# Kernel tuning notes

Hardware: AMD Instinct MI355X
Metric: run time of the kernel (lower is better)

Reference implementation:

```python
import jax, jax.numpy as jnp
import numpy as np

N, B = 1024, 32
PEP_PAD, L, M, E, VOCAB = 3, 27, 34, 16, 26
CN, KS, OFFS = (128, 256, 256), (3, 5, 7), (2, 1, 0)
LIN = (512, 256)
BN_EPS = 1e-5


def _pe(length, d):
    pos = np.arange(length, dtype=np.float32)[:, None]
    div = np.exp(np.arange(0, d, 2, dtype=np.float32) * (-np.log(10000.0) / d))
    pe = np.zeros((length, d), np.float32)
    pe[:, 0::2] = np.sin(pos * div)
    pe[:, 1::2] = np.cos(pos * div)
    return jnp.asarray(pe)

PE_MHC = _pe(M, E)
PE_PEP = _pe(100, E)[: L - 2 * PEP_PAD]


def _bn(x, g, b):
    # inference-mode BatchNorm2d (running_mean=0, running_var=1)
    s = g / jnp.sqrt(1.0 + BN_EPS)
    return x * s[None, :, None, None] + b[None, :, None, None]


def _iconv(pep, mhc, W, b):
    # interaction conv: pep (N, Lin, E, S), mhc (N, M, E), W (C, K, M)
    # out[n,c,i,s] = sum_{k,m,e} W[c,k,m] * mhc[n,m,e] * pep[n,i+k,e,s] + b[c]
    K = W.shape[1]
    Kb = jnp.einsum('ckm,nme->ncke', W, mhc)  # per-sample kernel (N,C,K,E)
    Lout = pep.shape[1] - K + 1
    out = sum(jnp.einsum('nce,nies->ncis', Kb[:, :, k], pep[:, k:k + Lout]) for k in range(K))
    return out + b[None, :, None, None]


def _fwd(params, peptide_x, mhc_x, bags_size, inverse):
    (emb_pep, emb_mhc, convs_f, convs_r, lins_f, lins_r,
     w_att1, b_att1, w_att2, b_att2, w_out, b_out) = params
    masks = peptide_x[:, PEP_PAD:L - PEP_PAD] != 0              # (N, 21)
    mhc_e = emb_mhc[mhc_x] + PE_MHC                             # (N, 34, E)
    pep_e = emb_pep[peptide_x]
    pep_e = jnp.concatenate([pep_e[:, :PEP_PAD],
                             pep_e[:, PEP_PAD:L - PEP_PAD] + PE_PEP,
                             pep_e[:, L - PEP_PAD:]], axis=1)    # (N, 27, E)
    pep_c = pep_e[..., None]                                     # (N,27,E,1)
    pep_i = jnp.stack([pep_e[:, ::-1], pep_e], axis=-1)          # (N,27,E,2)

    def branch(pep, convs, inversion):
        outs = []
        for (W, bb, g, be), off in zip(convs, OFFS):
            Wk = W[:, ::-1] if inversion else W
            x = _iconv(pep[:, off:L - off], mhc_e, Wk, bb)
            outs.append(jax.nn.relu(_bn(x, g, be)))
        return jnp.concatenate(outs, axis=1)

    conv_out = branch(pep_c, convs_f, False)                     # (N, 640, 21, 1)
    conv_r = branch(pep_i, convs_r, True)                        # (N, 640, 21, 2)
    conv_r = jnp.concatenate([conv_r[..., 0:1][:, :, ::-1], conv_r[..., 1:2]], axis=-1)

    def mlp(x, lins):
        for Wl, bl, gl, bel in lins:
            x = jax.nn.relu(_bn(jnp.einsum('oc,nciw->noiw', Wl, x) + bl[None, :, None, None], gl, bel))
        return x

    conv_out = mlp(conv_out, lins_f)                             # (N, 256, 21, 1)
    conv_r = mlp(conv_r, lins_r)                                 # (N, 256, 21, 2)
    x = jnp.concatenate([conv_out, conv_r], axis=-1)             # (N, 256, 21, 3)
    m = masks[:, None, -x.shape[2]:, None]
    pool = jnp.max(jnp.where(m, x, -jnp.inf), axis=2, keepdims=True)  # (N,256,1,3)

    # attention MIL over variable-size bags (segment softmax)
    feat = pool.mean(axis=(2, 3))                                # (N, 256)
    a = (jnp.tanh(feat @ w_att1.T + b_att1) @ w_att2.T + b_att2)[:, 0]
    nb = bags_size.shape[0]
    seg = jnp.repeat(jnp.arange(nb), bags_size, total_repeat_length=feat.shape[0])
    amax = jax.lax.stop_gradient(jax.ops.segment_max(a, seg, num_segments=nb))
    ex = jnp.exp(a - amax[seg])
    att = ex / jax.ops.segment_sum(ex, seg, num_segments=nb)[seg]

    score = jax.nn.sigmoid(jnp.einsum('oc,nciw->noiw', w_out, pool) + b_out[None, :, None, None])  # (N,2,1,3)
    half = score[..., :2].sum(-1) * 0.5
    if inverse:
        s = jnp.stack([half, score[..., -1]], axis=-1)           # (N,2,1,2)
    else:
        s = jnp.stack([half, half], axis=-1)
    s = s.max(axis=-1)                                           # (N, 2, 1)
    if inverse:
        s = jax.ops.segment_sum(att[:, None, None] * s, seg, num_segments=nb)  # (B,2,1)
    else:
        s = s.sum(axis=-1) * 0.5
    s = jnp.clip(s, 0.0, 1.0)
    return s.reshape(s.shape[0], -1)                             # (B, 2)


def setup_inputs() -> dict:
    key = jax.random.key(0)
    ks = iter(jax.random.split(key, 64))
    nrm = lambda shape, std=0.02: jax.random.normal(next(ks), shape, jnp.float32) * std
    d = {}
    d['peptide_x'] = jax.random.randint(next(ks), (N, L), 1, VOCAB)
    d['mhc_x'] = jax.random.randint(next(ks), (N, M), 1, VOCAB)
    d['context_x'] = jax.random.randint(next(ks), (N, 12), 1, VOCAB)
    d['peptide_esm_x'] = jnp.zeros((N, 2, 10, 3), jnp.float32)
    d['bags_size'] = jnp.full((B,), N // B, jnp.int32)
    d['inverse'] = 1
    d['emb_pep'] = jax.random.uniform(next(ks), (VOCAB, E), jnp.float32, -0.1, 0.1)
    d['emb_mhc'] = jax.random.uniform(next(ks), (VOCAB, E), jnp.float32, -0.1, 0.1)
    for tag in ('cf', 'cr'):
        for j, (c, k) in enumerate(zip(CN, KS)):
            d[f'w_{tag}{j}'] = nrm((c, k, M), 0.05)
            d[f'b_{tag}{j}'] = jnp.zeros((c,), jnp.float32)
            d[f'g_{tag}{j}'] = 1.0 + nrm((c,), 0.002)
            d[f'be_{tag}{j}'] = jnp.zeros((c,), jnp.float32)
    dims = [sum(CN)] + list(LIN)
    for tag in ('lf', 'lr'):
        for j, (i_s, o_s) in enumerate(zip(dims[:-1], dims[1:])):
            d[f'w_{tag}{j}'] = nrm((o_s, i_s), 0.02)
            d[f'b_{tag}{j}'] = jnp.zeros((o_s,), jnp.float32)
            d[f'g_{tag}{j}'] = 1.0 + nrm((o_s,), 0.002)
            d[f'be_{tag}{j}'] = jnp.zeros((o_s,), jnp.float32)
    H = LIN[-1]
    d['w_att1'] = nrm((H, H)); d['b_att1'] = jnp.zeros((H,), jnp.float32)
    d['w_att2'] = nrm((1, H)); d['b_att2'] = jnp.zeros((1,), jnp.float32)
    d['w_out'] = nrm((2, H), 0.1); d['b_out'] = jnp.zeros((2,), jnp.float32)
    return d


def reference(peptide_x, mhc_x, context_x, peptide_esm_x, bags_size, inverse,
              emb_pep, emb_mhc,
              w_cf0, b_cf0, g_cf0, be_cf0, w_cf1, b_cf1, g_cf1, be_cf1, w_cf2, b_cf2, g_cf2, be_cf2,
              w_cr0, b_cr0, g_cr0, be_cr0, w_cr1, b_cr1, g_cr1, be_cr1, w_cr2, b_cr2, g_cr2, be_cr2,
              w_lf0, b_lf0, g_lf0, be_lf0, w_lf1, b_lf1, g_lf1, be_lf1,
              w_lr0, b_lr0, g_lr0, be_lr0, w_lr1, b_lr1, g_lr1, be_lr1,
              w_att1, b_att1, w_att2, b_att2, w_out, b_out):
    convs_f = [(w_cf0, b_cf0, g_cf0, be_cf0), (w_cf1, b_cf1, g_cf1, be_cf1), (w_cf2, b_cf2, g_cf2, be_cf2)]
    convs_r = [(w_cr0, b_cr0, g_cr0, be_cr0), (w_cr1, b_cr1, g_cr1, be_cr1), (w_cr2, b_cr2, g_cr2, be_cr2)]
    lins_f = [(w_lf0, b_lf0, g_lf0, be_lf0), (w_lf1, b_lf1, g_lf1, be_lf1)]
    lins_r = [(w_lr0, b_lr0, g_lr0, be_lr0), (w_lr1, b_lr1, g_lr1, be_lr1)]
    params = (emb_pep, emb_mhc, convs_f, convs_r, lins_f, lins_r,
              w_att1, b_att1, w_att2, b_att2, w_out, b_out)
    return _fwd(params, peptide_x, mhc_x, bags_size, int(inverse))
```

## Files before the change

kernel.cpp:

```cpp
#include <hip/hip_runtime.h>
#include <hip/hip_bf16.h>
#include <math.h>

#define NS   1024
#define LP   27
#define MMH  34
#define EE   16
#define LO   21
#define CT   640
#define H1   512
#define H2   256
#define LPAD 40
#define GROW (LP*LPAD)
#define SLOTROWS (NS*LO)
#define ALLROWS  (3*SLOTROWS)

typedef __attribute__((ext_vector_type(8))) short  s8v;
typedef __attribute__((ext_vector_type(4))) float  f4v;

#define PK2_SLOT 147456
#define PK2_J0   0
#define PK2_J1   16384
#define PK2_J2   73728
#define WMLP_FAM 458752
#define WMLP_B   327680
#define BMLP_FAM 768
#define BMLP_B   512

__device__ __forceinline__ ushort f2b(float v) {
    __hip_bfloat16 hb = __float2bfloat16(v);
    return *reinterpret_cast<ushort*>(&hb);
}

__device__ __forceinline__ float pe_val(int pos, int e) {
    int j = e >> 1;
    float div = expf(-1.1512925464970229f * (float)j);
    float ang = (float)pos * div;
    return (e & 1) ? cosf(ang) : sinf(ang);
}

__device__ __forceinline__ int xcd_swz() {
    int fid = blockIdx.y * gridDim.x + blockIdx.x;
    int nwg = gridDim.x * gridDim.y;
    int cpx = nwg >> 3;
    return (fid & 7) * cpx + (fid >> 3);
}

struct PrepArgs {
    const int* pep_x; const int* mhc_x;
    const float* emb_pep; const float* emb_mhc;
    const float* cw[2][3]; const float* cb[2][3]; const float* cg[2][3]; const float* cbe[2][3];
    const float* mw[4]; const float* mb[4]; const float* mg[4]; const float* mbe[4];
    ushort* Gb; ushort* Wpack; float* bpack; ushort* Wmlp; float* bmlp; int* poolI;
};

__global__ __launch_bounds__(256) void k_prep(PrepArgs A) {
    int b = blockIdx.x, t = threadIdx.x;
    float rs = rsqrtf(1.0f + 1e-5f);
    if (b < NS) {
        __shared__ float ps[LP * 17];
        __shared__ float ms[MMH * 17];
        int n = b;
        for (int idx = t; idx < LP * EE; idx += 256) {
            int l = idx >> 4, e = idx & 15;
            float v = A.emb_pep[A.pep_x[n * LP + l] * EE + e];
            if (l >= 3 && l < 24) v += pe_val(l - 3, e);
            ps[l * 17 + e] = v;
        }
        for (int idx = t; idx < MMH * EE; idx += 256) {
            int m = idx >> 4, e = idx & 15;
            ms[m * 17 + e] = A.emb_mhc[A.mhc_x[n * MMH + m] * EE + e] + pe_val(m, e);
        }
        __syncthreads();
        for (int idx = t; idx < GROW; idx += 256) {
            int l = idx / LPAD, m = idx - l * LPAD;
            float s = 0.f;
            if (m < MMH) {
                #pragma unroll
                for (int e = 0; e < EE; ++e) s = fmaf(ps[l * 17 + e], ms[m * 17 + e], s);
            }
            A.Gb[(size_t)n * GROW + idx] = f2b(s);
        }
        if (n == 0 && t < 64) A.Gb[(size_t)NS * GROW + t] = 0;
    } else if (b < NS + 144) {
        const int KS_[3]  = {3, 5, 7};
        const int KCP_[3] = {128, 224, 288};
        const int NC_[3]  = {128, 256, 256};
        const int pkoff[3] = {PK2_J0, PK2_J1, PK2_J2};
        const int bpoff[3] = {0, 128, 384};
        int lin = b - NS;
        int s = lin / 48, rem = lin - s * 48, j = rem >> 4, z = rem & 15;
        int K = KS_[j], Kcp = KCP_[j], nc = NC_[j];
        int fam = (s == 0) ? 0 : 1;
        const float* w  = A.cw[fam][j];
        const float* g  = A.cg[fam][j];
        ushort* Wp = A.Wpack + s * PK2_SLOT + pkoff[j];
        int tot = nc * Kcp;
        for (int idx = z * 256 + t; idx < tot; idx += 16 * 256) {
            int c = idx / Kcp, col = idx - c * Kcp;
            int k = col / LPAD, m = col - k * LPAD;
            float v = 0.f;
            if (k < K && m < MMH) {
                int kk = (s == 2) ? (K - 1 - k) : k;
                v = w[((size_t)c * K + kk) * MMH + m] * (g[c] * rs);
            }
            Wp[idx] = f2b(v);
        }
        if (z == 0) {
            const float* bb = A.cb[fam][j];
            const float* be = A.cbe[fam][j];
            float* bp = A.bpack + s * CT + bpoff[j];
            for (int c = t; c < nc; c += 256)
                bp[c] = bb[c] * (g[c] * rs) + be[c];
        }
    } else if (b < NS + 144 + 112) {
        int lin = b - NS - 144;
        int task, rel, nb;
        if (lin < 40)      { task = 0; rel = lin;      nb = 40; }
        else if (lin < 56) { task = 1; rel = lin - 40; nb = 16; }
        else if (lin < 96) { task = 2; rel = lin - 56; nb = 40; }
        else               { task = 3; rel = lin - 96; nb = 16; }
        int fam = task >> 1, stage = task & 1;
        int Co = stage ? H2 : H1;
        int Ci = stage ? H1 : CT;
        const float* w  = A.mw[task];
        const float* g  = A.mg[task];
        ushort* Wb = A.Wmlp + fam * WMLP_FAM + stage * WMLP_B;
        int tot = Co * Ci;
        for (int idx = rel * 256 + t; idx < tot; idx += nb * 256) {
            int o = idx / Ci;
            Wb[idx] = f2b(w[idx] * (g[o] * rs));
        }
        if (rel == 0) {
            const float* bb = A.mb[task];
            const float* be = A.mbe[task];
            float* bp = A.bmlp + fam * BMLP_FAM + stage * BMLP_B;
            for (int o = t; o < Co; o += 256)
                bp[o] = bb[o] * (g[o] * rs) + be[o];
        }
    } else {
        int base = (b - NS - 144 - 112) * 8192;
        #pragma unroll
        for (int q = 0; q < 32; ++q)
            A.poolI[base + q * 256 + t] = 0;
    }
}

__global__ __launch_bounds__(512) void k_cmfma(
    const ushort* __restrict__ Gb, const ushort* __restrict__ Wpack,
    const float* __restrict__ bpack, ushort* __restrict__ Xb, int rowBase)
{
    const int kcpm[5] = {128, 224, 224, 288, 288};
    const int offm[5] = {2, 1, 1, 0, 0};
    const int o0m[5]  = {0, 0, 128, 0, 128};
    const int c0m[5]  = {0, 128, 128, 384, 384};
    const int wofm[5] = {PK2_J0, PK2_J1, PK2_J1, PK2_J2, PK2_J2};

    __shared__ ushort smC[17408];
    ushort* Al = smC;
    ushort* Bl = smC + 5120;
    int wg = xcd_swz();
    int y = wg % 5, rtile = wg / 5;
    int Kcp = kcpm[y], off = offm[y], o0 = o0m[y];
    int c0X = c0m[y] + o0;
    int r0g = rowBase + rtile * 128;
    int slot = r0g / SLOTROWS;
    const ushort* Wt = Wpack + slot * PK2_SLOT + wofm[y] + (size_t)o0 * Kcp;
    const float*  bp = bpack + slot * CT;
    int p0 = rtile * 128;

    int t = threadIdx.x, lane = t & 63, wv = t >> 6;
    int r0 = (wv >> 1) * 32, c0w = (wv & 1) * 64;

    int row_a = t >> 2, seg = t & 3;
    int rg0 = r0g + row_a;
    int rr0 = rg0 - slot * SLOTROWS;
    size_t wb0 = (size_t)(rr0 / LO) * GROW + (off + rr0 % LO) * LPAD;

    f4v acc[2][4];
    #pragma unroll
    for (int m = 0; m < 2; ++m)
        #pragma unroll
        for (int n = 0; n < 4; ++n)
            acc[m][n] = (f4v){0.f, 0.f, 0.f, 0.f};

    int nkt = Kcp >> 5;
    for (int kt = 0; kt < nkt; ++kt) {
        int k0 = kt << 5;
        __syncthreads();
        *(s8v*)&Al[row_a * 40 + seg * 8] = *(const s8v*)&Gb[wb0 + k0 + seg * 8];
        *(s8v*)&Bl[row_a * 40 + seg * 8] = *(const s8v*)&Wt[(size_t)row_a * Kcp + k0 + seg * 8];
        __syncthreads();
        s8v a[2], b[4];
        #pragma unroll
        for (int m = 0; m < 2; ++m)
            a[m] = *(const s8v*)&Al[(r0 + m * 16 + (lane & 15)) * 40 + (lane >> 4) * 8];
        #pragma unroll
        for (int n = 0; n < 4; ++n)
            b[n] = *(const s8v*)&Bl[(c0w + n * 16 + (lane & 15)) * 40 + (lane >> 4) * 8];
        #pragma unroll
        for (int m = 0; m < 2; ++m)
            #pragma unroll
            for (int n = 0; n < 4; ++n)
                acc[m][n] = __builtin_amdgcn_mfma_f32_16x16x32_bf16(a[m], b[n], acc[m][n], 0, 0, 0);
    }

    int cl = lane & 15, rq = lane >> 4;
    __syncthreads();
    #pragma unroll
    for (int m = 0; m < 2; ++m)
        #pragma unroll
        for (int n = 0; n < 4; ++n) {
            int ocr = c0w + n * 16 + cl;
            float bv = bp[c0X + ocr];
            #pragma unroll
            for (int j = 0; j < 4; ++j)
                smC[(r0 + m * 16 + rq * 4 + j) * 136 + ocr] = f2b(fmaxf(acc[m][n][j] + bv, 0.f));
        }
    __syncthreads();
    int ci = t & 15;
    #pragma unroll
    for (int it = 0; it < 4; ++it) {
        int row = (t >> 4) + it * 32;
        *(s8v*)&Xb[(size_t)(p0 + row) * CT + c0X + ci * 8] = *(const s8v*)&smC[row * 136 + ci * 8];
    }
}

__global__ __launch_bounds__(512) void k_mgemmA(
    const ushort* __restrict__ Xin,
    const ushort* __restrict__ Wbase, const float* __restrict__ bbase,
    ushort* __restrict__ Yb, int rowBase)
{
    __shared__ ushort smA[18432];
    ushort* Al = smA;
    ushort* Bl = smA + 9216;
    int t = threadIdx.x;
    int wg = xcd_swz();
    int o0 = (wg & 3) * 128;
    int p0 = (wg >> 2) * 128;
    int g0 = rowBase + p0;
    int fam = (g0 < SLOTROWS) ? 0 : 1;
    const ushort* Wb = Wbase + (size_t)fam * WMLP_FAM;
    const float*  bp = bbase + fam * BMLP_FAM;
    int lane = t & 63, wv = t >> 6;
    int r0 = (wv >> 1) * 32, c0 = (wv & 1) * 64;

    f4v acc[2][4];
    #pragma unroll
    for (int m = 0; m < 2; ++m)
        #pragma unroll
        for (int n = 0; n < 4; ++n)
            acc[m][n] = (f4v){0.f, 0.f, 0.f, 0.f};

    for (int kt = 0; kt < CT / 64; ++kt) {
        int k0 = kt << 6;
        __syncthreads();
        #pragma unroll
        for (int it = 0; it < 2; ++it) {
            int idx = t + it * 512;
            int row = idx >> 3, sg = idx & 7;
            *(s8v*)&Al[row * 72 + sg * 8] = *(const s8v*)&Xin[(size_t)(p0 + row) * CT + k0 + sg * 8];
            *(s8v*)&Bl[row * 72 + sg * 8] = *(const s8v*)&Wb[(size_t)(o0 + row) * CT + k0 + sg * 8];
        }
        __syncthreads();
        #pragma unroll
        for (int ks = 0; ks < 2; ++ks) {
            int kc = ks * 32 + (lane >> 4) * 8;
            s8v a[2], b[4];
            #pragma unroll
            for (int m = 0; m < 2; ++m)
                a[m] = *(const s8v*)&Al[(r0 + m * 16 + (lane & 15)) * 72 + kc];
            #pragma unroll
            for (int n = 0; n < 4; ++n)
                b[n] = *(const s8v*)&Bl[(c0 + n * 16 + (lane & 15)) * 72 + kc];
            #pragma unroll
            for (int m = 0; m < 2; ++m)
                #pragma unroll
                for (int n = 0; n < 4; ++n)
                    acc[m][n] = __builtin_amdgcn_mfma_f32_16x16x32_bf16(a[m], b[n], acc[m][n], 0, 0, 0);
        }
    }

    int cl = lane & 15, rq = lane >> 4;
    __syncthreads();
    #pragma unroll
    for (int m = 0; m < 2; ++m)
        #pragma unroll
        for (int n = 0; n < 4; ++n) {
            int ocr = c0 + n * 16 + cl;
            float bv = bp[o0 + ocr];
            #pragma unroll
            for (int j = 0; j < 4; ++j)
                smA[(r0 + m * 16 + rq * 4 + j) * 136 + ocr] = f2b(fmaxf(acc[m][n][j] + bv, 0.f));
        }
    __syncthreads();
    int ci = t & 15;
    #pragma unroll
    for (int it = 0; it < 4; ++it) {
        int row = (t >> 4) + it * 32;
        *(s8v*)&Yb[(size_t)(p0 + row) * H1 + o0 + ci * 8] = *(const s8v*)&smA[row * 136 + ci * 8];
    }
}

__global__ __launch_bounds__(512) void k_mgemmB(
    const ushort* __restrict__ Yin,
    const ushort* __restrict__ Wbase, const float* __restrict__ bbase,
    const int* __restrict__ pep_x, int* __restrict__ poolI, int rowBase)
{
    __shared__ float zbuf[128 * 129];
    __shared__ int mvalid[128];
    ushort* Al = (ushort*)zbuf;
    ushort* Bl = Al + 9216;
    int t = threadIdx.x;
    int wg = xcd_swz();
    int o0 = (wg & 1) * 128;
    int p0 = (wg >> 1) * 128;
    int g0 = rowBase + p0;
    int slot = g0 / SLOTROWS;
    int gs0 = g0 - slot * SLOTROWS;
    int fam = (slot == 0) ? 0 : 1;
    const ushort* Wb = Wbase + (size_t)fam * WMLP_FAM + WMLP_B;
    const float*  bp = bbase + fam * BMLP_FAM + BMLP_B;
    int lane = t & 63, wv = t >> 6;
    int r0 = (wv >> 1) * 32, c0 = (wv & 1) * 64;

    f4v acc[2][4];
    #pragma unroll
    for (int m = 0; m < 2; ++m)
        #pragma unroll
        for (int n = 0; n < 4; ++n)
            acc[m][n] = (f4v){0.f, 0.f, 0.f, 0.f};

    for (int kt = 0; kt < H1 / 64; ++kt) {
        int k0 = kt << 6;
        __syncthreads();
        #pragma unroll
        for (int it = 0; it < 2; ++it) {
            int idx = t + it * 512;
            int row = idx >> 3, sg = idx & 7;
            *(s8v*)&Al[row * 72 + sg * 8] = *(const s8v*)&Yin[(size_t)(p0 + row) * H1 + k0 + sg * 8];
            *(s8v*)&Bl[row * 72 + sg * 8] = *(const s8v*)&Wb[(size_t)(o0 + row) * H1 + k0 + sg * 8];
        }
        __syncthreads();
        #pragma unroll
        for (int ks = 0; ks < 2; ++ks) {
            int kc = ks * 32 + (lane >> 4) * 8;
            s8v a[2], b[4];
            #pragma unroll
            for (int m = 0; m < 2; ++m)
                a[m] = *(const s8v*)&Al[(r0 + m * 16 + (lane & 15)) * 72 + kc];
            #pragma unroll
            for (int n = 0; n < 4; ++n)
                b[n] = *(const s8v*)&Bl[(c0 + n * 16 + (lane & 15)) * 72 + kc];
            #pragma unroll
            for (int m = 0; m < 2; ++m)
                #pragma unroll
                for (int n = 0; n < 4; ++n)
                    acc[m][n] = __builtin_amdgcn_mfma_f32_16x16x32_bf16(a[m], b[n], acc[m][n], 0, 0, 0);
        }
    }

    int cl = lane & 15, rq = lane >> 4;
    __syncthreads();
    if (t < 128) {
        int gs = gs0 + t;
        int n = gs / LO, i = gs - n * LO;
        mvalid[t] = (pep_x[n * LP + 3 + i] != 0) ? 1 : 0;
    }
    #pragma unroll
    for (int m = 0; m < 2; ++m)
        #pragma unroll
        for (int n = 0; n < 4; ++n) {
            int ocr = c0 + n * 16 + cl;
            float bv = bp[o0 + ocr];
            #pragma unroll
            for (int j = 0; j < 4; ++j)
                zbuf[(r0 + m * 16 + rq * 4 + j) * 129 + ocr] = fmaxf(acc[m][n][j] + bv, 0.f);
        }
    __syncthreads();

    int col = t & 127, quart = t >> 7;
    int colg = o0 + col;
    int rs = quart * 32;
    int gs = gs0 + rs;
    int n = gs / LO, i = gs - n * LO;
    float cur = -1.f;
    for (int r = rs; r < rs + 32; ++r) {
        if (mvalid[r]) cur = fmaxf(cur, zbuf[r * 129 + col]);
        if (++i == LO) {
            if (cur >= 0.f)
                atomicMax(&poolI[n * (3 * H2) + slot * H2 + colg], __float_as_int(cur));
            cur = -1.f; ++n; i = 0;
        }
    }
    if (cur >= 0.f)
        atomicMax(&poolI[n * (3 * H2) + slot * H2 + colg], __float_as_int(cur));
}

__global__ __launch_bounds__(256) void k_poolhead(
    const float* __restrict__ pool,
    const float* __restrict__ w_att1, const float* __restrict__ b_att1,
    const float* __restrict__ w_att2, const float* __restrict__ b_att2,
    const float* __restrict__ w_out, const float* __restrict__ b_out,
    float* __restrict__ a_out, float* __restrict__ s2_out)
{
    int n = blockIdx.x, c = threadIdx.x;
    __shared__ float feat_s[H2];
    __shared__ float red[7][H2];
    __shared__ float sc_s[6];

    float mx[3];
    #pragma unroll
    for (int w = 0; w < 3; ++w)
        mx[w] = pool[(size_t)n * (3 * H2) + w * H2 + c];

    float fv = (mx[0] + mx[1] + mx[2]) * (1.f / 3.f);
    feat_s[c] = fv;
    #pragma unroll
    for (int o = 0; o < 2; ++o)
        #pragma unroll
        for (int w = 0; w < 3; ++w)
            red[o * 3 + w][c] = w_out[o * H2 + c] * mx[w];
    __syncthreads();

    float hacc = 0.f;
    for (int cc = 0; cc < H2; ++cc)
        hacc = fmaf(w_att1[(size_t)c * H2 + cc], feat_s[cc], hacc);
    float h = tanhf(hacc + b_att1[c]);
    red[6][c] = h * w_att2[c];
    __syncthreads();

    for (int s = 128; s > 0; s >>= 1) {
        if (c < s) {
            #pragma unroll
            for (int jj = 0; jj < 7; ++jj) red[jj][c] += red[jj][c + s];
        }
        __syncthreads();
    }
    if (c == 0) a_out[n] = red[6][0] + b_att2[0];
    if (c < 6) {
        float x = red[c][0] + b_out[c / 3];
        sc_s[c] = 1.f / (1.f + expf(-x));
    }
    __syncthreads();
    if (c < 2) {
        float half = 0.5f * (sc_s[c * 3 + 0] + sc_s[c * 3 + 1]);
        s2_out[n * 2 + c] = fmaxf(half, sc_s[c * 3 + 2]);
    }
}

__global__ __launch_bounds__(1024) void k_final(
    const float* __restrict__ a_in, const float* __restrict__ s2_in,
    const int* __restrict__ bags, float* __restrict__ out)
{
    __shared__ float a_s[NS], s0_s[NS], s1_s[NS];
    __shared__ int off_s[33];
    int t = threadIdx.x;
    a_s[t]  = a_in[t];
    s0_s[t] = s2_in[t * 2 + 0];
    s1_s[t] = s2_in[t * 2 + 1];
    if (t == 0) {
        off_s[0] = 0;
        for (int g = 0; g < 32; ++g) off_s[g + 1] = off_s[g] + bags[g];
    }
    __syncthreads();
    if (t < 32) {
        int st = off_s[t], en = off_s[t + 1];
        float mxv = -INFINITY;
        for (int n = st; n < en; ++n) mxv = fmaxf(mxv, a_s[n]);
        float se = 0.f;
        for (int n = st; n < en; ++n) se += expf(a_s[n] - mxv);
        float inv = 1.f / se;
        float o0 = 0.f, o1 = 0.f;
        for (int n = st; n < en; ++n) {
            float w = expf(a_s[n] - mxv) * inv;
            o0 += w * s0_s[n];
            o1 += w * s1_s[n];
        }
        out[t * 2 + 0] = fminf(fmaxf(o0, 0.f), 1.f);
        out[t * 2 + 1] = fminf(fmaxf(o1, 0.f), 1.f);
    }
}

extern "C" void kernel_launch(void* const* d_in, const int* in_sizes, int n_in,
                              void* d_out, int out_size, void* d_ws, size_t ws_size,
                              hipStream_t stream) {
    const int* pep_x = (const int*)d_in[0];
    const int* mhc_x = (const int*)d_in[1];
    const int* bags  = (const int*)d_in[4];

    char* wsb = (char*)d_ws;
    float*  pool   = (float*) (wsb + 0);
    int*    poolI  = (int*)   (wsb + 0);
    float*  a_buf  = (float*) (wsb + 3145728);
    float*  s2_buf = (float*) (wsb + 3149824);
    ushort* Wpack  = (ushort*)(wsb + 3158016);
    float*  bpack  = (float*) (wsb + 4042752);
    ushort* Wmlp   = (ushort*)(wsb + 4050432);
    float*  bmlp   = (float*) (wsb + 5885440);
    ushort* Gb     = (ushort*)(wsb + 5891584);
    const size_t XB_B = 8103552;

    size_t fullNeed = XB_B + (size_t)ALLROWS * (1280 + 1024);
    int chunkSlots = (fullNeed <= ws_size) ? 3 : 1;
    int RC = chunkSlots * SLOTROWS;
    ushort* Xb = (ushort*)(wsb + XB_B);
    ushort* Yb = (ushort*)((char*)Xb + (size_t)RC * 1280);

    PrepArgs pa;
    pa.pep_x = pep_x; pa.mhc_x = mhc_x;
    pa.emb_pep = (const float*)d_in[6];
    pa.emb_mhc = (const float*)d_in[7];
    for (int j = 0; j < 3; ++j) {
        pa.cw[0][j]  = (const float*)d_in[8 + 4 * j];
        pa.cb[0][j]  = (const float*)d_in[9 + 4 * j];
        pa.cg[0][j]  = (const float*)d_in[10 + 4 * j];
        pa.cbe[0][j] = (const float*)d_in[11 + 4 * j];
        pa.cw[1][j]  = (const float*)d_in[20 + 4 * j];
        pa.cb[1][j]  = (const float*)d_in[21 + 4 * j];
        pa.cg[1][j]  = (const float*)d_in[22 + 4 * j];
        pa.cbe[1][j] = (const float*)d_in[23 + 4 * j];
    }
    for (int task = 0; task < 4; ++task) {
        int base = 32 + task * 4;
        pa.mw[task]  = (const float*)d_in[base + 0];
        pa.mb[task]  = (const float*)d_in[base + 1];
        pa.mg[task]  = (const float*)d_in[base + 2];
        pa.mbe[task] = (const float*)d_in[base + 3];
    }
    pa.Gb = Gb; pa.Wpack = Wpack; pa.bpack = bpack; pa.Wmlp = Wmlp; pa.bmlp = bmlp;
    pa.poolI = poolI;

    k_prep<<<dim3(NS + 144 + 112 + 96), dim3(256), 0, stream>>>(pa);

    for (int rowBase = 0; rowBase < ALLROWS; rowBase += RC) {
        int nRB = RC / 128;
        k_cmfma<<<dim3(5, nRB), dim3(512), 0, stream>>>(Gb, Wpack, bpack, Xb, rowBase);
        k_mgemmA<<<dim3(H1 / 128, nRB), dim3(512), 0, stream>>>(Xb, Wmlp, bmlp, Yb, rowBase);
        k_mgemmB<<<dim3(H2 / 128, nRB), dim3(512), 0, stream>>>(Yb, Wmlp, bmlp, pep_x, poolI, rowBase);
    }

    k_poolhead<<<dim3(NS), dim3(256), 0, stream>>>(
        pool,
        (const float*)d_in[48], (const float*)d_in[49], (const float*)d_in[50], (const float*)d_in[51],
        (const float*)d_in[52], (const float*)d_in[53],
        a_buf, s2_buf);

    k_final<<<dim3(1), dim3(1024), 0, stream>>>(a_buf, s2_buf, bags, (float*)d_out);
}
```

Baseline: 189.6 us.

## Double-buffer GEMM tiles via direct global-to-LDS loads in conv and MLP kernels

Replaces the register-staged global->LDS tile copies in the three MFMA GEMM kernels with global_load_lds direct transfers into a double-buffered, k-chunk-major LDS layout. The next k-tile is prefetched while the current one feeds MFMAs, with explicit vmcnt waits and raw s_barriers in place of syncthreads. This is meant to hide global load latency and remove the VGPR round-trip. The cost is doubled LDS footprint and a new unpadded layout that may cause bank conflicts on the fragment reads.

```diff
diff --git a/kernel.cpp b/kernel.cpp
--- a/kernel.cpp
+++ b/kernel.cpp
@@ -37,6 +37,12 @@
     float div = expf(-1.1512925464970229f * (float)j);
     float ang = (float)pos * div;
     return (e & 1) ? cosf(ang) : sinf(ang);
+}
+
+__device__ __forceinline__ void gl16(const ushort* g, ushort* l) {
+    __builtin_amdgcn_global_load_lds(
+        (const __attribute__((address_space(1))) void*)g,
+        (__attribute__((address_space(3))) void*)l, 16, 0, 0);
 }
 
 __device__ __forceinline__ int xcd_swz() {
@@ -157,8 +163,6 @@
     const int wofm[5] = {PK2_J0, PK2_J1, PK2_J1, PK2_J2, PK2_J2};
 
     __shared__ ushort smC[17408];
-    ushort* Al = smC;
-    ushort* Bl = smC + 5120;
     int wg = xcd_swz();
     int y = wg % 5, rtile = wg / 5;
     int Kcp = kcpm[y], off = offm[y], o0 = o0m[y];
@@ -172,10 +176,25 @@
     int t = threadIdx.x, lane = t & 63, wv = t >> 6;
     int r0 = (wv >> 1) * 32, c0w = (wv & 1) * 64;
 
-    int row_a = t >> 2, seg = t & 3;
-    int rg0 = r0g + row_a;
-    int rr0 = rg0 - slot * SLOTROWS;
-    size_t wb0 = (size_t)(rr0 / LO) * GROW + (off + rr0 % LO) * LPAD;
+    const ushort* sb0; const ushort* sb1; int lo0, lo1;
+    {
+        int isB = wv >= 4;
+        int kb  = isB ? (wv - 4) : wv;
+        #pragma unroll
+        for (int i = 0; i < 2; ++i) {
+            int hf = i, row = hf * 64 + lane;
+            const ushort* s;
+            if (isB) {
+                s = Wt + (size_t)row * Kcp + kb * 8;
+            } else {
+                int rg = r0g + row;
+                int rr = rg - slot * SLOTROWS;
+                s = Gb + (size_t)(rr / LO) * GROW + (off + rr % LO) * LPAD + kb * 8;
+            }
+            int lo = (isB ? 4096 : 0) + kb * 1024 + hf * 512;
+            if (i == 0) { sb0 = s; lo0 = lo; } else { sb1 = s; lo1 = lo; }
+        }
+    }
 
     f4v acc[2][4];
     #pragma unroll
@@ -185,28 +204,40 @@
             acc[m][n] = (f4v){0.f, 0.f, 0.f, 0.f};
 
     int nkt = Kcp >> 5;
+    gl16(sb0, &smC[lo0]);
+    gl16(sb1, &smC[lo1]);
     for (int kt = 0; kt < nkt; ++kt) {
-        int k0 = kt << 5;
-        __syncthreads();
-        *(s8v*)&Al[row_a * 40 + seg * 8] = *(const s8v*)&Gb[wb0 + k0 + seg * 8];
-        *(s8v*)&Bl[row_a * 40 + seg * 8] = *(const s8v*)&Wt[(size_t)row_a * Kcp + k0 + seg * 8];
-        __syncthreads();
+        if (kt + 1 < nkt) {
+            int nb = ((kt + 1) & 1) << 13;
+            int ko = (kt + 1) * 32;
+            gl16(sb0 + ko, &smC[nb + lo0]);
+            gl16(sb1 + ko, &smC[nb + lo1]);
+            asm volatile("s_waitcnt vmcnt(2)" ::: "memory");
+        } else {
+            asm volatile("s_waitcnt vmcnt(0)" ::: "memory");
+        }
+        __builtin_amdgcn_sched_barrier(0);
+        __builtin_amdgcn_s_barrier();
+        __builtin_amdgcn_sched_barrier(0);
+        int cb = (kt & 1) << 13;
+        int kq = (lane >> 4) * 128;
         s8v a[2], b[4];
         #pragma unroll
         for (int m = 0; m < 2; ++m)
-            a[m] = *(const s8v*)&Al[(r0 + m * 16 + (lane & 15)) * 40 + (lane >> 4) * 8];
+            a[m] = *(const s8v*)&smC[cb + (kq + r0 + m * 16 + (lane & 15)) * 8];
         #pragma unroll
         for (int n = 0; n < 4; ++n)
-            b[n] = *(const s8v*)&Bl[(c0w + n * 16 + (lane & 15)) * 40 + (lane >> 4) * 8];
+            b[n] = *(const s8v*)&smC[cb + 4096 + (kq + c0w + n * 16 + (lane & 15)) * 8];
         #pragma unroll
         for (int m = 0; m < 2; ++m)
             #pragma unroll
             for (int n = 0; n < 4; ++n)
                 acc[m][n] = __builtin_amdgcn_mfma_f32_16x16x32_bf16(a[m], b[n], acc[m][n], 0, 0, 0);
+        __builtin_amdgcn_sched_barrier(0);
+        __builtin_amdgcn_s_barrier();
     }
 
     int cl = lane & 15, rq = lane >> 4;
-    __syncthreads();
     #pragma unroll
     for (int m = 0; m < 2; ++m)
         #pragma unroll
@@ -231,9 +262,7 @@
     const ushort* __restrict__ Wbase, const float* __restrict__ bbase,
     ushort* __restrict__ Yb, int rowBase)
 {
-    __shared__ ushort smA[18432];
-    ushort* Al = smA;
-    ushort* Bl = smA + 9216;
+    __shared__ ushort smA[32768];
     int t = threadIdx.x;
     int wg = xcd_swz();
     int o0 = (wg & 3) * 128;
@@ -245,6 +274,17 @@
     int lane = t & 63, wv = t >> 6;
     int r0 = (wv >> 1) * 32, c0 = (wv & 1) * 64;
 
+    const ushort* sb[4]; int lo[4];
+    #pragma unroll
+    for (int i = 0; i < 4; ++i) {
+        int c = wv * 4 + i;
+        int isB = c >= 16;
+        int cc = c & 15, kb = cc >> 1, hf = cc & 1;
+        int row = hf * 64 + lane;
+        sb[i] = (isB ? Wb + (size_t)(o0 + row) * CT : Xin + (size_t)(p0 + row) * CT) + kb * 8;
+        lo[i] = (isB ? 8192 : 0) + kb * 1024 + hf * 512;
+    }
+
     f4v acc[2][4];
     #pragma unroll
     for (int m = 0; m < 2; ++m)
@@ -252,37 +292,44 @@
         for (int n = 0; n < 4; ++n)
             acc[m][n] = (f4v){0.f, 0.f, 0.f, 0.f};
 
-    for (int kt = 0; kt < CT / 64; ++kt) {
-        int k0 = kt << 6;
-        __syncthreads();
-        #pragma unroll
-        for (int it = 0; it < 2; ++it) {
-            int idx = t + it * 512;
-            int row = idx >> 3, sg = idx & 7;
-            *(s8v*)&Al[row * 72 + sg * 8] = *(const s8v*)&Xin[(size_t)(p0 + row) * CT + k0 + sg * 8];
-            *(s8v*)&Bl[row * 72 + sg * 8] = *(const s8v*)&Wb[(size_t)(o0 + row) * CT + k0 + sg * 8];
-        }
-        __syncthreads();
+    const int NKT = CT / 64;
+    #pragma unroll
+    for (int i = 0; i < 4; ++i) gl16(sb[i], &smA[lo[i]]);
+    for (int kt = 0; kt < NKT; ++kt) {
+        if (kt + 1 < NKT) {
+            int nb = ((kt + 1) & 1) << 14;
+            int ko = (kt + 1) * 64;
+            #pragma unroll
+            for (int i = 0; i < 4; ++i) gl16(sb[i] + ko, &smA[nb + lo[i]]);
+            asm volatile("s_waitcnt vmcnt(4)" ::: "memory");
+        } else {
+            asm volatile("s_waitcnt vmcnt(0)" ::: "memory");
+        }
+        __builtin_amdgcn_sched_barrier(0);
+        __builtin_amdgcn_s_barrier();
+        __builtin_amdgcn_sched_barrier(0);
+        int cb = (kt & 1) << 14;
         #pragma unroll
         for (int ks = 0; ks < 2; ++ks) {
-            int kc = ks * 32 + (lane >> 4) * 8;
+            int kq = (ks * 4 + (lane >> 4)) * 128;
             s8v a[2], b[4];
             #pragma unroll
             for (int m = 0; m < 2; ++m)
-                a[m] = *(const s8v*)&Al[(r0 + m * 16 + (lane & 15)) * 72 + kc];
+                a[m] = *(const s8v*)&smA[cb + (kq + r0 + m * 16 + (lane & 15)) * 8];
             #pragma unroll
             for (int n = 0; n < 4; ++n)
-                b[n] = *(const s8v*)&Bl[(c0 + n * 16 + (lane & 15)) * 72 + kc];
+                b[n] = *(const s8v*)&smA[cb + 8192 + (kq + c0 + n * 16 + (lane & 15)) * 8];
             #pragma unroll
             for (int m = 0; m < 2; ++m)
                 #pragma unroll
                 for (int n = 0; n < 4; ++n)
                     acc[m][n] = __builtin_amdgcn_mfma_f32_16x16x32_bf16(a[m], b[n], acc[m][n], 0, 0, 0);
         }
+        __builtin_amdgcn_sched_barrier(0);
+        __builtin_amdgcn_s_barrier();
     }
 
     int cl = lane & 15, rq = lane >> 4;
-    __syncthreads();
     #pragma unroll
     for (int m = 0; m < 2; ++m)
         #pragma unroll
@@ -307,10 +354,9 @@
     const ushort* __restrict__ Wbase, const float* __restrict__ bbase,
     const int* __restrict__ pep_x, int* __restrict__ poolI, int rowBase)
 {
-    __shared__ float zbuf[128 * 129];
+    __shared__ float zbuf[16512];
     __shared__ int mvalid[128];
-    ushort* Al = (ushort*)zbuf;
-    ushort* Bl = Al + 9216;
+    ushort* smB = (ushort*)zbuf;
     int t = threadIdx.x;
     int wg = xcd_swz();
     int o0 = (wg & 1) * 128;
@@ -324,6 +370,17 @@
     int lane = t & 63, wv = t >> 6;
     int r0 = (wv >> 1) * 32, c0 = (wv & 1) * 64;
 
+    const ushort* sb[4]; int lo[4];
+    #pragma unroll
+    for (int i = 0; i < 4; ++i) {
+        int c = wv * 4 + i;
+        int isB = c >= 16;
+        int cc = c & 15, kb = cc >> 1, hf = cc & 1;
+        int row = hf * 64 + lane;
+        sb[i] = (isB ? Wb + (size_t)(o0 + row) * H1 : Yin + (size_t)(p0 + row) * H1) + kb * 8;
+        lo[i] = (isB ? 8192 : 0) + kb * 1024 + hf * 512;
+    }
+
     f4v acc[2][4];
     #pragma unroll
     for (int m = 0; m < 2; ++m)
@@ -331,37 +388,44 @@
         for (int n = 0; n < 4; ++n)
             acc[m][n] = (f4v){0.f, 0.f, 0.f, 0.f};
 
-    for (int kt = 0; kt < H1 / 64; ++kt) {
-        int k0 = kt << 6;
-        __syncthreads();
-        #pragma unroll
-        for (int it = 0; it < 2; ++it) {
-            int idx = t + it * 512;
-            int row = idx >> 3, sg = idx & 7;
-            *(s8v*)&Al[row * 72 + sg * 8] = *(const s8v*)&Yin[(size_t)(p0 + row) * H1 + k0 + sg * 8];
-            *(s8v*)&Bl[row * 72 + sg * 8] = *(const s8v*)&Wb[(size_t)(o0 + row) * H1 + k0 + sg * 8];
-        }
-        __syncthreads();
+    const int NKT = H1 / 64;
+    #pragma unroll
+    for (int i = 0; i < 4; ++i) gl16(sb[i], &smB[lo[i]]);
+    for (int kt = 0; kt < NKT; ++kt) {
+        if (kt + 1 < NKT) {
+            int nb = ((kt + 1) & 1) << 14;
+            int ko = (kt + 1) * 64;
+            #pragma unroll
+            for (int i = 0; i < 4; ++i) gl16(sb[i] + ko, &smB[nb + lo[i]]);
+            asm volatile("s_waitcnt vmcnt(4)" ::: "memory");
+        } else {
+            asm volatile("s_waitcnt vmcnt(0)" ::: "memory");
+        }
+        __builtin_amdgcn_sched_barrier(0);
+        __builtin_amdgcn_s_barrier();
+        __builtin_amdgcn_sched_barrier(0);
+        int cb = (kt & 1) << 14;
         #pragma unroll
         for (int ks = 0; ks < 2; ++ks) {
-            int kc = ks * 32 + (lane >> 4) * 8;
+            int kq = (ks * 4 + (lane >> 4)) * 128;
             s8v a[2], b[4];
             #pragma unroll
             for (int m = 0; m < 2; ++m)
-                a[m] = *(const s8v*)&Al[(r0 + m * 16 + (lane & 15)) * 72 + kc];
+                a[m] = *(const s8v*)&smB[cb + (kq + r0 + m * 16 + (lane & 15)) * 8];
             #pragma unroll
             for (int n = 0; n < 4; ++n)
-                b[n] = *(const s8v*)&Bl[(c0 + n * 16 + (lane & 15)) * 72 + kc];
+                b[n] = *(const s8v*)&smB[cb + 8192 + (kq + c0 + n * 16 + (lane & 15)) * 8];
             #pragma unroll
             for (int m = 0; m < 2; ++m)
                 #pragma unroll
                 for (int n = 0; n < 4; ++n)
                     acc[m][n] = __builtin_amdgcn_mfma_f32_16x16x32_bf16(a[m], b[n], acc[m][n], 0, 0, 0);
         }
+        __builtin_amdgcn_sched_barrier(0);
+        __builtin_amdgcn_s_barrier();
     }
 
     int cl = lane & 15, rq = lane >> 4;
-    __syncthreads();
     if (t < 128) {
         int gs = gs0 + t;
         int n = gs / LO, i = gs - n * LO;
```

Result: slower. 215.2 us (+13.5%).

## Load MFMA operands directly from global memory, bypassing LDS staging in GEMM kernels

Applied to the files above, without the earlier changes.

All three MFMA GEMM kernels (interaction conv, MLP layer A, MLP layer B) now give each lane precomputed pointers and load its A/B fragments straight from global memory into registers. This replaces the shared-memory tile staging and its two barriers per k-step. The k loop is unrolled by four so independent loads can overlap with MFMAs. The cost is lost data reuse across waves: each tile is fetched by several waves through the cache rather than once into LDS, which raises global/L2 traffic.

```diff
diff --git a/kernel.cpp b/kernel.cpp
--- a/kernel.cpp
+++ b/kernel.cpp
@@ -157,8 +157,6 @@
     const int wofm[5] = {PK2_J0, PK2_J1, PK2_J1, PK2_J2, PK2_J2};
 
     __shared__ ushort smC[17408];
-    ushort* Al = smC;
-    ushort* Bl = smC + 5120;
     int wg = xcd_swz();
     int y = wg % 5, rtile = wg / 5;
     int Kcp = kcpm[y], off = offm[y], o0 = o0m[y];
@@ -171,11 +169,19 @@
 
     int t = threadIdx.x, lane = t & 63, wv = t >> 6;
     int r0 = (wv >> 1) * 32, c0w = (wv & 1) * 64;
-
-    int row_a = t >> 2, seg = t & 3;
-    int rg0 = r0g + row_a;
-    int rr0 = rg0 - slot * SLOTROWS;
-    size_t wb0 = (size_t)(rr0 / LO) * GROW + (off + rr0 % LO) * LPAD;
+    int lr = lane & 15, kq = lane >> 4;
+
+    const ushort* aP[2];
+    const ushort* bP[4];
+    #pragma unroll
+    for (int m = 0; m < 2; ++m) {
+        int rg = r0g + r0 + m * 16 + lr;
+        int rr = rg - slot * SLOTROWS;
+        aP[m] = Gb + (size_t)(rr / LO) * GROW + (off + rr % LO) * LPAD + kq * 8;
+    }
+    #pragma unroll
+    for (int n = 0; n < 4; ++n)
+        bP[n] = Wt + (size_t)(c0w + n * 16 + lr) * Kcp + kq * 8;
 
     f4v acc[2][4];
     #pragma unroll
@@ -185,19 +191,14 @@
             acc[m][n] = (f4v){0.f, 0.f, 0.f, 0.f};
 
     int nkt = Kcp >> 5;
+    #pragma unroll 4
     for (int kt = 0; kt < nkt; ++kt) {
         int k0 = kt << 5;
-        __syncthreads();
-        *(s8v*)&Al[row_a * 40 + seg * 8] = *(const s8v*)&Gb[wb0 + k0 + seg * 8];
-        *(s8v*)&Bl[row_a * 40 + seg * 8] = *(const s8v*)&Wt[(size_t)row_a * Kcp + k0 + seg * 8];
-        __syncthreads();
         s8v a[2], b[4];
         #pragma unroll
-        for (int m = 0; m < 2; ++m)
-            a[m] = *(const s8v*)&Al[(r0 + m * 16 + (lane & 15)) * 40 + (lane >> 4) * 8];
-        #pragma unroll
-        for (int n = 0; n < 4; ++n)
-            b[n] = *(const s8v*)&Bl[(c0w + n * 16 + (lane & 15)) * 40 + (lane >> 4) * 8];
+        for (int m = 0; m < 2; ++m) a[m] = *(const s8v*)(aP[m] + k0);
+        #pragma unroll
+        for (int n = 0; n < 4; ++n) b[n] = *(const s8v*)(bP[n] + k0);
         #pragma unroll
         for (int m = 0; m < 2; ++m)
             #pragma unroll
@@ -206,7 +207,6 @@
     }
 
     int cl = lane & 15, rq = lane >> 4;
-    __syncthreads();
     #pragma unroll
     for (int m = 0; m < 2; ++m)
         #pragma unroll
@@ -231,9 +231,7 @@
     const ushort* __restrict__ Wbase, const float* __restrict__ bbase,
     ushort* __restrict__ Yb, int rowBase)
 {
-    __shared__ ushort smA[18432];
-    ushort* Al = smA;
-    ushort* Bl = smA + 9216;
+    __shared__ ushort smA[17408];
     int t = threadIdx.x;
     int wg = xcd_swz();
     int o0 = (wg & 3) * 128;
@@ -244,6 +242,16 @@
     const float*  bp = bbase + fam * BMLP_FAM;
     int lane = t & 63, wv = t >> 6;
     int r0 = (wv >> 1) * 32, c0 = (wv & 1) * 64;
+    int lr = lane & 15, kq = lane >> 4;
+
+    const ushort* aP[2];
+    const ushort* bP[4];
+    #pragma unroll
+    for (int m = 0; m < 2; ++m)
+        aP[m] = Xin + (size_t)(p0 + r0 + m * 16 + lr) * CT + kq * 8;
+    #pragma unroll
+    for (int n = 0; n < 4; ++n)
+        bP[n] = Wb + (size_t)(o0 + c0 + n * 16 + lr) * CT + kq * 8;
 
     f4v acc[2][4];
     #pragma unroll
@@ -252,37 +260,22 @@
         for (int n = 0; n < 4; ++n)
             acc[m][n] = (f4v){0.f, 0.f, 0.f, 0.f};
 
-    for (int kt = 0; kt < CT / 64; ++kt) {
-        int k0 = kt << 6;
-        __syncthreads();
-        #pragma unroll
-        for (int it = 0; it < 2; ++it) {
-            int idx = t + it * 512;
-            int row = idx >> 3, sg = idx & 7;
-            *(s8v*)&Al[row * 72 + sg * 8] = *(const s8v*)&Xin[(size_t)(p0 + row) * CT + k0 + sg * 8];
-            *(s8v*)&Bl[row * 72 + sg * 8] = *(const s8v*)&Wb[(size_t)(o0 + row) * CT + k0 + sg * 8];
-        }
-        __syncthreads();
-        #pragma unroll
-        for (int ks = 0; ks < 2; ++ks) {
-            int kc = ks * 32 + (lane >> 4) * 8;
-            s8v a[2], b[4];
-            #pragma unroll
-            for (int m = 0; m < 2; ++m)
-                a[m] = *(const s8v*)&Al[(r0 + m * 16 + (lane & 15)) * 72 + kc];
+    #pragma unroll 4
+    for (int kt = 0; kt < CT / 32; ++kt) {
+        int k0 = kt << 5;
+        s8v a[2], b[4];
+        #pragma unroll
+        for (int m = 0; m < 2; ++m) a[m] = *(const s8v*)(aP[m] + k0);
+        #pragma unroll
+        for (int n = 0; n < 4; ++n) b[n] = *(const s8v*)(bP[n] + k0);
+        #pragma unroll
+        for (int m = 0; m < 2; ++m)
             #pragma unroll
             for (int n = 0; n < 4; ++n)
-                b[n] = *(const s8v*)&Bl[(c0 + n * 16 + (lane & 15)) * 72 + kc];
-            #pragma unroll
-            for (int m = 0; m < 2; ++m)
-                #pragma unroll
-                for (int n = 0; n < 4; ++n)
-                    acc[m][n] = __builtin_amdgcn_mfma_f32_16x16x32_bf16(a[m], b[n], acc[m][n], 0, 0, 0);
-        }
+                acc[m][n] = __builtin_amdgcn_mfma_f32_16x16x32_bf16(a[m], b[n], acc[m][n], 0, 0, 0);
     }
 
     int cl = lane & 15, rq = lane >> 4;
-    __syncthreads();
     #pragma unroll
     for (int m = 0; m < 2; ++m)
         #pragma unroll
@@ -309,8 +302,6 @@
 {
     __shared__ float zbuf[128 * 129];
     __shared__ int mvalid[128];
-    ushort* Al = (ushort*)zbuf;
-    ushort* Bl = Al + 9216;
     int t = threadIdx.x;
     int wg = xcd_swz();
     int o0 = (wg & 1) * 128;
@@ -323,6 +314,16 @@
     const float*  bp = bbase + fam * BMLP_FAM + BMLP_B;
     int lane = t & 63, wv = t >> 6;
     int r0 = (wv >> 1) * 32, c0 = (wv & 1) * 64;
+    int lr = lane & 15, kq = lane >> 4;
+
+    const ushort* aP[2];
+    const ushort* bP[4];
+    #pragma unroll
+    for (int m = 0; m < 2; ++m)
+        aP[m] = Yin + (size_t)(p0 + r0 + m * 16 + lr) * H1 + kq * 8;
+    #pragma unroll
+    for (int n = 0; n < 4; ++n)
+        bP[n] = Wb + (size_t)(o0 + c0 + n * 16 + lr) * H1 + kq * 8;
 
     f4v acc[2][4];
     #pragma unroll
@@ -331,37 +332,22 @@
         for (int n = 0; n < 4; ++n)
             acc[m][n] = (f4v){0.f, 0.f, 0.f, 0.f};
 
-    for (int kt = 0; kt < H1 / 64; ++kt) {
-        int k0 = kt << 6;
-        __syncthreads();
-        #pragma unroll
-        for (int it = 0; it < 2; ++it) {
-            int idx = t + it * 512;
-            int row = idx >> 3, sg = idx & 7;
-            *(s8v*)&Al[row * 72 + sg * 8] = *(const s8v*)&Yin[(size_t)(p0 + row) * H1 + k0 + sg * 8];
-            *(s8v*)&Bl[row * 72 + sg * 8] = *(const s8v*)&Wb[(size_t)(o0 + row) * H1 + k0 + sg * 8];
-        }
-        __syncthreads();
-        #pragma unroll
-        for (int ks = 0; ks < 2; ++ks) {
-            int kc = ks * 32 + (lane >> 4) * 8;
-            s8v a[2], b[4];
-            #pragma unroll
-            for (int m = 0; m < 2; ++m)
-                a[m] = *(const s8v*)&Al[(r0 + m * 16 + (lane & 15)) * 72 + kc];
+    #pragma unroll 4
+    for (int kt = 0; kt < H1 / 32; ++kt) {
+        int k0 = kt << 5;
+        s8v a[2], b[4];
+        #pragma unroll
+        for (int m = 0; m < 2; ++m) a[m] = *(const s8v*)(aP[m] + k0);
+        #pragma unroll
+        for (int n = 0; n < 4; ++n) b[n] = *(const s8v*)(bP[n] + k0);
+        #pragma unroll
+        for (int m = 0; m < 2; ++m)
             #pragma unroll
             for (int n = 0; n < 4; ++n)
-                b[n] = *(const s8v*)&Bl[(c0 + n * 16 + (lane & 15)) * 72 + kc];
-            #pragma unroll
-            for (int m = 0; m < 2; ++m)
-                #pragma unroll
-                for (int n = 0; n < 4; ++n)
-                    acc[m][n] = __builtin_amdgcn_mfma_f32_16x16x32_bf16(a[m], b[n], acc[m][n], 0, 0, 0);
-        }
+                acc[m][n] = __builtin_amdgcn_mfma_f32_16x16x32_bf16(a[m], b[n], acc[m][n], 0, 0, 0);
     }
 
     int cl = lane & 15, rq = lane >> 4;
-    __syncthreads();
     if (t < 128) {
         int gs = gs0 + t;
         int n = gs / LO, i = gs - n * LO;
```

Result: slower. 422.1 us (+122.6%).
